# Performance work log

Hardware: AMD Instinct MI355X
Metric: run time of the kernel (lower is better)

The kernel has to match this reference:

```python
import jax, jax.numpy as jnp
import numpy as np

G = 64      # num graphs
N = 1024    # nodes per graph (equal-sized graphs)
D_IN, D_H, D_OUT = 128, 256, 10


def setup_inputs() -> dict:
    key = jax.random.key(0)
    k1, k2, k3, k4, k5 = jax.random.split(key, 5)
    x = jax.random.normal(k1, (G * N, D_IN), dtype=jnp.float32)
    batch = jnp.repeat(jnp.arange(G, dtype=jnp.int64), N)  # sorted graph ids
    lim1 = 1.0 / np.sqrt(D_IN)
    lim2 = 1.0 / np.sqrt(D_H)
    W1 = jax.random.uniform(k2, (D_IN, D_H), minval=-lim1, maxval=lim1, dtype=jnp.float32)
    b1 = jax.random.uniform(k3, (D_H,), minval=-lim1, maxval=lim1, dtype=jnp.float32)
    W2 = jax.random.uniform(k4, (D_H, D_OUT), minval=-lim2, maxval=lim2, dtype=jnp.float32)
    b2 = jax.random.uniform(k5, (D_OUT,), minval=-lim2, maxval=lim2, dtype=jnp.float32)
    return {"x": x, "batch": batch, "W1": W1, "b1": b1, "W2": W2, "b2": b2}


def reference(x, batch, W1, b1, W2, b2):
    # Equal-sized graphs: reshape node dim into [G, N, d] (batch is sorted).
    xg = x.reshape(G, N, D_IN)
    # Cosine-similarity adjacency per graph, zero diagonal (from RAW features).
    xn = xg * jax.lax.rsqrt(jnp.sum(xg * xg, axis=-1, keepdims=True) + 1e-24)
    adj = jnp.einsum('gnd,gmd->gnm', xn, xn)            # [G, N, N]
    adj = adj * (1.0 - jnp.eye(N, dtype=adj.dtype))
    # fc1 + relu on node features, then adjacency propagation.
    h = jax.nn.relu(xg @ W1 + b1)                       # [G, N, D_H]
    h = jnp.einsum('gnm,gmd->gnd', adj, h)              # [G, N, D_H]
    # fc2, global mean pool over nodes, log-softmax over classes.
    out = h @ W2 + b2                                   # [G, N, D_OUT]
    pooled = jnp.mean(out, axis=1)                      # [G, D_OUT]
    return jax.nn.log_softmax(pooled, axis=-1)
```

## Files before the change

kernel.cpp:

```cpp
#include <hip/hip_runtime.h>

#define G_ 64
#define N_ 1024
#define DIN 128
#define DH 256
#define DOUT 10

typedef float floatx4 __attribute__((ext_vector_type(4)));
typedef short shortx8 __attribute__((ext_vector_type(8)));

__device__ __forceinline__ ushort f2bf(float f) {
  unsigned u = __builtin_bit_cast(unsigned, f);
  unsigned r = (u + 0x7FFFu + ((u >> 16) & 1u)) >> 16;
  return (ushort)r;
}

__device__ __forceinline__ unsigned cvtpk(float a, float b) {
  unsigned r;
  asm("v_cvt_pk_bf16_f32 %0, %1, %2" : "=v"(r) : "v"(a), "v"(b));
  return r;
}

__global__ __launch_bounds__(256) void k1(
    const float* __restrict__ x, const float* __restrict__ W1,
    ushort* __restrict__ w1t, float* __restrict__ u_part,
    float* __restrict__ norminv) {
  const int bid = blockIdx.x;
  const int tid = threadIdx.x;
  const int wave = tid >> 6;
  const int lane = tid & 63;
  const int half = lane >> 5;
  const int l32 = lane & 31;
  const int m0 = bid << 6;

  __shared__ float red[8][DIN];

  if (bid < DIN)
    w1t[(size_t)tid * DIN + bid] = f2bf(W1[(size_t)bid * DH + tid]);

  float a0 = 0.f, a1 = 0.f, a2 = 0.f, a3 = 0.f;
  #pragma unroll
  for (int it = 0; it < 8; ++it) {
    const int m = m0 + (wave << 4) + (it << 1) + half;
    const float4 v = ((const float4*)(x + (size_t)m * DIN))[l32];
    float ss = v.x * v.x + v.y * v.y + v.z * v.z + v.w * v.w;
    #pragma unroll
    for (int off = 16; off; off >>= 1) ss += __shfl_xor(ss, off, 64);
    const float ninv = rsqrtf(ss + 1e-24f);
    if (l32 == 0) norminv[m] = ninv;
    a0 = fmaf(v.x, ninv, a0);
    a1 = fmaf(v.y, ninv, a1);
    a2 = fmaf(v.z, ninv, a2);
    a3 = fmaf(v.w, ninv, a3);
  }
  float4 av; av.x = a0; av.y = a1; av.z = a2; av.w = a3;
  ((float4*)red[(wave << 1) + half])[l32] = av;
  __syncthreads();
  if (tid < DIN) {
    float s = 0.f;
    #pragma unroll
    for (int i = 0; i < 8; ++i) s += red[i][tid];
    u_part[bid * DIN + tid] = s;
  }
}

__global__ __launch_bounds__(256) void k2(
    const float* __restrict__ x, const ushort* __restrict__ w1t,
    const float* __restrict__ b1, const float* __restrict__ u_part,
    const float* __restrict__ norminv, float* __restrict__ hw_part) {
  const int bid = blockIdx.x;
  const int tid = threadIdx.x;
  const int wave = tid >> 6;
  const int lane = tid & 63;
  const int g = bid >> 3;
  const int m0 = bid << 7;
  const int quad = lane >> 4;
  const int l16 = lane & 15;

  __shared__ float u_lds[DIN];
  __shared__ float ninv_lds[128];

  if (tid < DIN) {
    float s = 0.f;
    #pragma unroll
    for (int i = 0; i < 16; ++i) s += u_part[((g << 4) + i) * DIN + tid];
    u_lds[tid] = s;
  } else {
    ninv_lds[tid - 128] = norminv[m0 + tid - 128];
  }
  __syncthreads();

  float uu[4][8];
  #pragma unroll
  for (int kt = 0; kt < 4; ++kt)
    #pragma unroll
    for (int j = 0; j < 8; ++j) uu[kt][j] = u_lds[(kt << 5) + (quad << 3) + j];

  shortx8 bfr[4][4];
  #pragma unroll
  for (int dt = 0; dt < 4; ++dt) {
    const int d = (wave << 6) + (dt << 4) + l16;
    #pragma unroll
    for (int kt = 0; kt < 4; ++kt)
      bfr[dt][kt] =
          *(const shortx8*)(w1t + (size_t)d * DIN + (kt << 5) + (quad << 3));
  }
  float b1v[4];
  #pragma unroll
  for (int dt = 0; dt < 4; ++dt) b1v[dt] = b1[(wave << 6) + (dt << 4) + l16];

  float wsum[4] = {0.f, 0.f, 0.f, 0.f};
  for (int mt = 0; mt < 8; ++mt) {
    const float4* xr =
        (const float4*)(x + ((size_t)m0 + (mt << 4) + l16) * DIN);
    shortx8 af[4];
    float p = 0.f;
    #pragma unroll
    for (int kt = 0; kt < 4; ++kt) {
      const float4 fa = xr[(kt << 3) + (quad << 1)];
      const float4 fb = xr[(kt << 3) + (quad << 1) + 1];
      const float* ub = uu[kt];
      p = fmaf(fa.x, ub[0], p); p = fmaf(fa.y, ub[1], p);
      p = fmaf(fa.z, ub[2], p); p = fmaf(fa.w, ub[3], p);
      p = fmaf(fb.x, ub[4], p); p = fmaf(fb.y, ub[5], p);
      p = fmaf(fb.z, ub[6], p); p = fmaf(fb.w, ub[7], p);
      uint4 pk;
      pk.x = cvtpk(fa.x, fa.y);
      pk.y = cvtpk(fa.z, fa.w);
      pk.z = cvtpk(fb.x, fb.y);
      pk.w = cvtpk(fb.z, fb.w);
      af[kt] = __builtin_bit_cast(shortx8, pk);
    }

    floatx4 acc[4] = {{0.f, 0.f, 0.f, 0.f}, {0.f, 0.f, 0.f, 0.f},
                      {0.f, 0.f, 0.f, 0.f}, {0.f, 0.f, 0.f, 0.f}};
    #pragma unroll
    for (int kt = 0; kt < 4; ++kt)
      #pragma unroll
      for (int dt = 0; dt < 4; ++dt)
        acc[dt] = __builtin_amdgcn_mfma_f32_16x16x32_bf16(af[kt], bfr[dt][kt],
                                                          acc[dt], 0, 0, 0);

    p += __shfl_xor(p, 16, 64);
    p += __shfl_xor(p, 32, 64);
    const float s_l = p * ninv_lds[(mt << 4) + l16] - 1.0f;

    float sv[4];
    #pragma unroll
    for (int r = 0; r < 4; ++r)
      sv[r] = __shfl(s_l, (lane & 48) | ((quad << 2) + r), 64);

    #pragma unroll
    for (int dt = 0; dt < 4; ++dt) {
      float bs = 0.f;
      #pragma unroll
      for (int r = 0; r < 4; ++r) {
        const float h = fmaxf(acc[dt][r] + b1v[dt], 0.f);
        bs = fmaf(sv[r], h, bs);
      }
      wsum[dt] += bs;
    }
  }
  #pragma unroll
  for (int dt = 0; dt < 4; ++dt) {
    float w = wsum[dt];
    w += __shfl_xor(w, 16, 64);
    w += __shfl_xor(w, 32, 64);
    if (quad == 0)
      hw_part[bid * DH + (wave << 6) + (dt << 4) + l16] = w;
  }
}

__global__ __launch_bounds__(256) void k3(
    const float* __restrict__ hw_part, const float* __restrict__ W2,
    const float* __restrict__ b2, float* __restrict__ out) {
  const int g = blockIdx.x;
  const int tid = threadIdx.x;
  __shared__ float hv[DH];
  __shared__ float partial[40];
  __shared__ float pv[DOUT];

  float h = 0.f;
  #pragma unroll
  for (int i = 0; i < 8; ++i) h += hw_part[((g << 3) + i) * DH + tid];
  hv[tid] = h;
  __syncthreads();
  if (tid < 40) {
    const int c = tid % 10, q = tid / 10;
    float a = 0.f;
    #pragma unroll
    for (int k = 0; k < 64; ++k)
      a = fmaf(hv[q * 64 + k], W2[(q * 64 + k) * DOUT + c], a);
    partial[tid] = a;
  }
  __syncthreads();
  if (tid < DOUT) {
    pv[tid] = (partial[tid] + partial[tid + 10] + partial[tid + 20] +
               partial[tid + 30]) * (1.0f / N_) + b2[tid];
  }
  __syncthreads();
  if (tid < DOUT) {
    float mx = pv[0];
    #pragma unroll
    for (int c = 1; c < DOUT; ++c) mx = fmaxf(mx, pv[c]);
    float se = 0.f;
    #pragma unroll
    for (int c = 0; c < DOUT; ++c) se += expf(pv[c] - mx);
    out[g * DOUT + tid] = pv[tid] - (mx + logf(se));
  }
}

extern "C" void kernel_launch(void* const* d_in, const int* in_sizes, int n_in,
                              void* d_out, int out_size, void* d_ws, size_t ws_size,
                              hipStream_t stream) {
  const float* x  = (const float*)d_in[0];
  const float* W1 = (const float*)d_in[2];
  const float* b1 = (const float*)d_in[3];
  const float* W2 = (const float*)d_in[4];
  const float* b2 = (const float*)d_in[5];
  float* out = (float*)d_out;

  ushort* w1t = (ushort*)d_ws;
  float* u_part  = (float*)(w1t + (size_t)DH * DIN);
  float* hw_part = u_part + (size_t)1024 * DIN;
  float* norminv = hw_part + (size_t)512 * DH;

  k1<<<1024, 256, 0, stream>>>(x, W1, w1t, u_part, norminv);
  k2<<<512, 256, 0, stream>>>(x, w1t, b1, u_part, norminv, hw_part);
  k3<<<G_, 256, 0, stream>>>(hw_part, W2, b2, out);
}
```

Baseline: 105.7 us.

## Compute node-sum dot products via split-bf16 MFMA and double k2 grid

The per-node dot product with the graph feature sum, previously done with scalar FMAs on fp32 x, now uses two extra MFMAs against the sum vector split into high and low bf16 parts (only column 0 nonzero). The result is broadcast by shuffle from the column-0 lanes. k2 also now processes 64 rows per block instead of 128 and launches 1024 blocks, so k3 sums 16 partials per graph and the workspace layout shifts. This offloads VALU work and raises parallelism, but x is now rounded to bf16 in the dot product, which costs accuracy, and it adds partial-sum traffic.

```diff
diff --git a/kernel.cpp b/kernel.cpp
--- a/kernel.cpp
+++ b/kernel.cpp
@@ -72,29 +72,39 @@
   const int tid = threadIdx.x;
   const int wave = tid >> 6;
   const int lane = tid & 63;
-  const int g = bid >> 3;
-  const int m0 = bid << 7;
+  const int g = bid >> 4;
+  const int m0 = bid << 6;
   const int quad = lane >> 4;
   const int l16 = lane & 15;
 
   __shared__ float u_lds[DIN];
-  __shared__ float ninv_lds[128];
+  __shared__ float ninv_lds[64];
 
   if (tid < DIN) {
     float s = 0.f;
     #pragma unroll
     for (int i = 0; i < 16; ++i) s += u_part[((g << 4) + i) * DIN + tid];
     u_lds[tid] = s;
-  } else {
+  } else if (tid < 192) {
     ninv_lds[tid - 128] = norminv[m0 + tid - 128];
   }
   __syncthreads();
 
-  float uu[4][8];
-  #pragma unroll
-  for (int kt = 0; kt < 4; ++kt)
-    #pragma unroll
-    for (int j = 0; j < 8; ++j) uu[kt][j] = u_lds[(kt << 5) + (quad << 3) + j];
+  shortx8 buh[4], bul[4];
+  #pragma unroll
+  for (int kt = 0; kt < 4; ++kt) {
+    shortx8 h, l;
+    #pragma unroll
+    for (int j = 0; j < 8; ++j) {
+      const float uv = (l16 == 0) ? u_lds[(kt << 5) + (quad << 3) + j] : 0.f;
+      const ushort uh = f2bf(uv);
+      const float uhf = __builtin_bit_cast(float, (unsigned)uh << 16);
+      h[j] = (short)uh;
+      l[j] = (short)f2bf(uv - uhf);
+    }
+    buh[kt] = h;
+    bul[kt] = l;
+  }
 
   shortx8 bfr[4][4];
   #pragma unroll
@@ -110,20 +120,14 @@
   for (int dt = 0; dt < 4; ++dt) b1v[dt] = b1[(wave << 6) + (dt << 4) + l16];
 
   float wsum[4] = {0.f, 0.f, 0.f, 0.f};
-  for (int mt = 0; mt < 8; ++mt) {
+  for (int mt = 0; mt < 4; ++mt) {
     const float4* xr =
         (const float4*)(x + ((size_t)m0 + (mt << 4) + l16) * DIN);
     shortx8 af[4];
-    float p = 0.f;
     #pragma unroll
     for (int kt = 0; kt < 4; ++kt) {
       const float4 fa = xr[(kt << 3) + (quad << 1)];
       const float4 fb = xr[(kt << 3) + (quad << 1) + 1];
-      const float* ub = uu[kt];
-      p = fmaf(fa.x, ub[0], p); p = fmaf(fa.y, ub[1], p);
-      p = fmaf(fa.z, ub[2], p); p = fmaf(fa.w, ub[3], p);
-      p = fmaf(fb.x, ub[4], p); p = fmaf(fb.y, ub[5], p);
-      p = fmaf(fb.z, ub[6], p); p = fmaf(fb.w, ub[7], p);
       uint4 pk;
       pk.x = cvtpk(fa.x, fa.y);
       pk.y = cvtpk(fa.z, fa.w);
@@ -134,21 +138,25 @@
 
     floatx4 acc[4] = {{0.f, 0.f, 0.f, 0.f}, {0.f, 0.f, 0.f, 0.f},
                       {0.f, 0.f, 0.f, 0.f}, {0.f, 0.f, 0.f, 0.f}};
-    #pragma unroll
-    for (int kt = 0; kt < 4; ++kt)
+    floatx4 accu = {0.f, 0.f, 0.f, 0.f};
+    #pragma unroll
+    for (int kt = 0; kt < 4; ++kt) {
       #pragma unroll
       for (int dt = 0; dt < 4; ++dt)
         acc[dt] = __builtin_amdgcn_mfma_f32_16x16x32_bf16(af[kt], bfr[dt][kt],
                                                           acc[dt], 0, 0, 0);
-
-    p += __shfl_xor(p, 16, 64);
-    p += __shfl_xor(p, 32, 64);
-    const float s_l = p * ninv_lds[(mt << 4) + l16] - 1.0f;
+      accu = __builtin_amdgcn_mfma_f32_16x16x32_bf16(af[kt], buh[kt], accu,
+                                                     0, 0, 0);
+      accu = __builtin_amdgcn_mfma_f32_16x16x32_bf16(af[kt], bul[kt], accu,
+                                                     0, 0, 0);
+    }
 
     float sv[4];
     #pragma unroll
-    for (int r = 0; r < 4; ++r)
-      sv[r] = __shfl(s_l, (lane & 48) | ((quad << 2) + r), 64);
+    for (int r = 0; r < 4; ++r) {
+      const float dot = __shfl(accu[r], lane & 48, 64);
+      sv[r] = dot * ninv_lds[(mt << 4) + (quad << 2) + r] - 1.0f;
+    }
 
     #pragma unroll
     for (int dt = 0; dt < 4; ++dt) {
@@ -182,7 +190,7 @@
 
   float h = 0.f;
   #pragma unroll
-  for (int i = 0; i < 8; ++i) h += hw_part[((g << 3) + i) * DH + tid];
+  for (int i = 0; i < 16; ++i) h += hw_part[((g << 4) + i) * DH + tid];
   hv[tid] = h;
   __syncthreads();
   if (tid < 40) {
@@ -223,9 +231,9 @@
   ushort* w1t = (ushort*)d_ws;
   float* u_part  = (float*)(w1t + (size_t)DH * DIN);
   float* hw_part = u_part + (size_t)1024 * DIN;
-  float* norminv = hw_part + (size_t)512 * DH;
+  float* norminv = hw_part + (size_t)1024 * DH;
 
   k1<<<1024, 256, 0, stream>>>(x, W1, w1t, u_part, norminv);
-  k2<<<512, 256, 0, stream>>>(x, w1t, b1, u_part, norminv, hw_part);
+  k2<<<1024, 256, 0, stream>>>(x, w1t, b1, u_part, norminv, hw_part);
   k3<<<G_, 256, 0, stream>>>(hw_part, W2, b2, out);
 }
```

New measurement: 114.1 us. 7.9% more time.
